# Kernel optimization log

Measured on AMD Instinct MI355X. Metric: run time of the kernel, lower is better.

The kernel has to match this reference:

```python
import jax, jax.numpy as jnp
import numpy as np
from jax import lax

IMG, P, L, H, D, MLPD, NC, B = 224, 16, 12, 12, 768, 3072, 1000, 32
G = IMG // P          # 14 patches per side
S = G * G + 1         # 197 tokens (class token + patches)
DH = D // H           # 64 head dim
EPS = 1e-6


def setup_inputs() -> dict:
    key = jax.random.key(0)
    ks = jax.random.split(key, 10)
    def nrm(k, shape, s=0.02):
        return jax.random.normal(k, shape, jnp.float32) * s
    return {
        "x": jax.random.normal(ks[0], (B, 3, IMG, IMG), jnp.float32),
        "tangent": jax.random.normal(ks[1], (B, 3, IMG, IMG), jnp.float32),
        "conv_w": nrm(ks[2], (D, 3, P, P)),
        "conv_b": jnp.zeros((D,), jnp.float32),
        "class_token": jnp.zeros((1, 1, D), jnp.float32),
        "pos_emb": nrm(ks[3], (1, S, D)),
        "ln1_g": jnp.ones((L, D), jnp.float32), "ln1_b": jnp.zeros((L, D), jnp.float32),
        "qkv_w": nrm(ks[4], (L, 3 * D, D)), "qkv_b": jnp.zeros((L, 3 * D), jnp.float32),
        "out_w": nrm(ks[5], (L, D, D)), "out_b": jnp.zeros((L, D), jnp.float32),
        "ln2_g": jnp.ones((L, D), jnp.float32), "ln2_b": jnp.zeros((L, D), jnp.float32),
        "fc1_w": nrm(ks[6], (L, MLPD, D)), "fc1_b": jnp.zeros((L, MLPD), jnp.float32),
        "fc2_w": nrm(ks[7], (L, D, MLPD)), "fc2_b": jnp.zeros((L, D), jnp.float32),
        "lnf_g": jnp.ones((D,), jnp.float32), "lnf_b": jnp.zeros((D,), jnp.float32),
        "head_w": nrm(ks[8], (NC, D)), "head_b": jnp.zeros((NC,), jnp.float32),
    }


def _layer_norm(x, g, b):
    mu = jnp.mean(x, -1, keepdims=True)
    var = jnp.mean(jnp.square(x - mu), -1, keepdims=True)
    return (x - mu) * lax.rsqrt(var + EPS) * g + b


def _vit(x, conv_w, conv_b, class_token, pos_emb, ln1_g, ln1_b, qkv_w, qkv_b,
         out_w, out_b, ln2_g, ln2_b, fc1_w, fc1_b, fc2_w, fc2_b, lnf_g, lnf_b,
         head_w, head_b):
    n = x.shape[0]
    # patch embedding == Conv2d(3, D, kernel=P, stride=P)
    xr = x.reshape(n, 3, G, P, G, P)
    tok = jnp.einsum('ncgphq,dcpq->nghd', xr, conv_w).reshape(n, G * G, D) + conv_b
    cls = jnp.broadcast_to(class_token, (n, 1, D))
    z = jnp.concatenate([cls, tok], axis=1) + pos_emb  # [n, S, D]

    def block(z, p):
        l1g, l1b, qw, qb, ow, ob, l2g, l2b, f1w, f1b, f2w, f2b = p
        y = _layer_norm(z, l1g, l1b)
        qkv = jnp.einsum('nsd,ed->nse', y, qw) + qb          # [n,S,3D]
        q, k, v = jnp.split(qkv, 3, axis=-1)
        q = q.reshape(n, S, H, DH).transpose(0, 2, 1, 3)
        k = k.reshape(n, S, H, DH).transpose(0, 2, 1, 3)
        v = v.reshape(n, S, H, DH).transpose(0, 2, 1, 3)
        scores = jnp.einsum('nhqd,nhkd->nhqk', q, k) / jnp.sqrt(jnp.float32(DH))
        a = jax.nn.softmax(scores, axis=-1)
        o = jnp.einsum('nhqk,nhkd->nhqd', a, v).transpose(0, 2, 1, 3).reshape(n, S, D)
        o = jnp.einsum('nsd,ed->nse', o, ow) + ob
        z = z + o
        y2 = _layer_norm(z, l2g, l2b)
        h = jax.nn.gelu(jnp.einsum('nsd,ed->nse', y2, f1w) + f1b, approximate=False)
        z = z + jnp.einsum('nse,de->nsd', h, f2w) + f2b
        return z, None

    z, _ = lax.scan(block, z, (ln1_g, ln1_b, qkv_w, qkv_b, out_w, out_b,
                               ln2_g, ln2_b, fc1_w, fc1_b, fc2_w, fc2_b))
    z = _layer_norm(z, lnf_g, lnf_b)
    return z[:, 0] @ head_w.T + head_b  # [n, NC]


def reference(x, tangent, conv_w, conv_b, class_token, pos_emb, ln1_g, ln1_b,
              qkv_w, qkv_b, out_w, out_b, ln2_g, ln2_b, fc1_w, fc1_b, fc2_w,
              fc2_b, lnf_g, lnf_b, head_w, head_b):
    f = lambda xx: _vit(xx, conv_w, conv_b, class_token, pos_emb, ln1_g, ln1_b,
                        qkv_w, qkv_b, out_w, out_b, ln2_g, ln2_b, fc1_w, fc1_b,
                        fc2_w, fc2_b, lnf_g, lnf_b, head_w, head_b)
    out, out_jvp = jax.jvp(f, (x,), (tangent,))
    return out, out_jvp
```

## Files before the change

kernel.cpp:

```cpp
#include <hip/hip_runtime.h>
#include <math.h>

static constexpr int B_   = 32;
static constexpr int S_   = 197;
static constexpr int D_   = 768;
static constexpr int H_   = 12;
static constexpr int L_   = 12;
static constexpr int MD_  = 3072;
static constexpr int NC_  = 1000;
static constexpr int GP_  = 196;
static constexpr int KP_  = 224;
static constexpr int MP_  = 6400;

typedef __attribute__((ext_vector_type(8))) short bf16x8v;
typedef __attribute__((ext_vector_type(4))) float f32x4v;

__device__ __forceinline__ unsigned short f2bf(float x) {
    union { float f; unsigned u; } v; v.f = x;
    unsigned r = v.u + 0x7fffu + ((v.u >> 16) & 1u);
    return (unsigned short)(r >> 16);
}

#define GLOAD_LDS16(gptr, lptr) \
    __builtin_amdgcn_global_load_lds((const __attribute__((address_space(1))) void*)(gptr), \
        (__attribute__((address_space(3))) void*)(lptr), 16, 0, 0)

template<int MODE, bool BIAS>
__global__ __launch_bounds__(512, 2) void mfma_pair_kernel(
    const short* __restrict__ Af, const short* __restrict__ At,
    const short* __restrict__ Bm, const float* __restrict__ bias,
    void* __restrict__ Cfv, void* __restrict__ Ctv,
    int Mhalf, int N, int K, int ldc)
{
    int bx, by;
    {
        const int gx = gridDim.x, nwg = gx * gridDim.y;
        const int flat = blockIdx.y * gx + blockIdx.x;
        const int q = nwg >> 3, r = nwg & 7;
        const int xcd = flat & 7, idx = flat >> 3;
        const int nf = (xcd < r ? xcd * (q + 1) : r * (q + 1) + (xcd - r) * q) + idx;
        bx = nf % gx; by = nf / gx;
    }
    __shared__ __align__(16) short ldsAf[2][128 * 32];
    __shared__ __align__(16) short ldsAt[2][128 * 32];
    __shared__ __align__(16) short ldsB [2][128 * 32];
    const int tid  = threadIdx.x;
    const int lane = tid & 63;
    const int w    = tid >> 6;
    const int m0 = by * 128, n0 = bx * 128;
    const int wr = w >> 1, wc = w & 1;
    f32x4v accf[2][4] = {}, acct[2][4] = {};

    const int r_in = lane >> 2;
    const int cdst = lane & 3;
    const int srow = w * 16 + r_in;
    const int csrc = cdst ^ ((srow >> 1) & 3);
    const size_t aoff = (size_t)(m0 + srow) * K + csrc * 8;
    const size_t boff = (size_t)(n0 + srow) * K + csrc * 8;

    GLOAD_LDS16(Af + aoff, &ldsAf[0][w * 512]);
    GLOAD_LDS16(At + aoff, &ldsAt[0][w * 512]);
    GLOAD_LDS16(Bm + boff, &ldsB [0][w * 512]);
    __syncthreads();

    int cur = 0;
    for (int k0 = 0; k0 < K; k0 += 32) {
        const int nxt = cur ^ 1;
        if (k0 + 32 < K) {
            GLOAD_LDS16(Af + aoff + k0 + 32, &ldsAf[nxt][w * 512]);
            GLOAD_LDS16(At + aoff + k0 + 32, &ldsAt[nxt][w * 512]);
            GLOAD_LDS16(Bm + boff + k0 + 32, &ldsB [nxt][w * 512]);
        }
        bf16x8v af[2], at[2], bfr[4];
        #pragma unroll
        for (int m = 0; m < 2; ++m) {
            const int row = wr * 32 + m * 16 + (lane & 15);
            const int c = (lane >> 4) ^ ((row >> 1) & 3);
            af[m] = *(const bf16x8v*)&ldsAf[cur][row * 32 + c * 8];
            at[m] = *(const bf16x8v*)&ldsAt[cur][row * 32 + c * 8];
        }
        #pragma unroll
        for (int n = 0; n < 4; ++n) {
            const int row = wc * 64 + n * 16 + (lane & 15);
            const int c = (lane >> 4) ^ ((row >> 1) & 3);
            bfr[n] = *(const bf16x8v*)&ldsB[cur][row * 32 + c * 8];
        }
        #pragma unroll
        for (int m = 0; m < 2; ++m)
            #pragma unroll
            for (int n = 0; n < 4; ++n) {
                accf[m][n] = __builtin_amdgcn_mfma_f32_16x16x32_bf16(af[m], bfr[n], accf[m][n], 0, 0, 0);
                acct[m][n] = __builtin_amdgcn_mfma_f32_16x16x32_bf16(at[m], bfr[n], acct[m][n], 0, 0, 0);
            }
        __syncthreads();
        cur = nxt;
    }
    const int col_base = n0 + wc * 64 + (lane & 15);
    const int row_base = m0 + wr * 32 + (lane >> 4) * 4;
    #pragma unroll
    for (int n = 0; n < 4; ++n) {
        const int col = col_base + n * 16;
        const float bv = BIAS ? bias[col] : 0.f;
        #pragma unroll
        for (int m = 0; m < 2; ++m) {
            const int row = row_base + m * 16;
            #pragma unroll
            for (int r = 0; r < 4; ++r) {
                if (row + r < Mhalf) {
                    const size_t off = (size_t)(row + r) * ldc + col;
                    const float vf = accf[m][n][r] + bv;
                    const float vt = acct[m][n][r];
                    if (MODE == 0) {
                        ((float*)Cfv)[off] = vf;
                        ((float*)Ctv)[off] = vt;
                    } else if (MODE == 1) {
                        ((float*)Cfv)[off] += vf;
                        ((float*)Ctv)[off] += vt;
                    } else if (MODE == 2) {
                        ((short*)Cfv)[off] = (short)f2bf(vf);
                        ((short*)Ctv)[off] = (short)f2bf(vt);
                    } else {
                        const float cdf = 0.5f * (1.0f + erff(vf * 0.70710678118654752f));
                        const float pdf = 0.3989422804014327f * expf(-0.5f * vf * vf);
                        ((short*)Cfv)[off] = (short)f2bf(vf * cdf);
                        ((short*)Ctv)[off] = (short)f2bf(vt * (cdf + vf * pdf));
                    }
                }
            }
        }
    }
}

__global__ __launch_bounds__(256) void attn_fused_kernel(
    const short* __restrict__ qkvb, const short* __restrict__ dqkvb,
    const short* __restrict__ Vtb_, const short* __restrict__ dVtb_,
    short* __restrict__ obf, short* __restrict__ dobf)
{
    const int qt = blockIdx.x;
    const int b  = blockIdx.y;
    const int n = b / H_, h = b - n * H_;
    const short* qb  = qkvb  + (size_t)n * S_ * 2304 + h * 64;
    const short* kb  = qb + 768;
    const short* dqb = dqkvb + (size_t)n * S_ * 2304 + h * 64;
    const short* dkb = dqb + 768;
    const short* Vb  = Vtb_  + (size_t)b * 64 * KP_;
    const short* dVb = dVtb_ + (size_t)b * 64 * KP_;

    __shared__ __align__(16) short lds[32768];
    const int tid = threadIdx.x, lane = tid & 63, w = tid >> 6;
    const int g = lane >> 4, kc = lane & 15;
    const int srow = lane >> 2, cdst = lane & 3;
    const int csrc = cdst ^ ((srow >> 1) & 3);

    {
        const size_t qr = (size_t)min(qt * 64 + w * 16 + srow, S_ - 1) * 2304;
        #pragma unroll
        for (int kw = 0; kw < 2; ++kw) {
            GLOAD_LDS16(qb  + qr + kw * 32 + csrc * 8, &lds[w * 1024 + kw * 512]);
            GLOAD_LDS16(dqb + qr + kw * 32 + csrc * 8, &lds[4096 + w * 1024 + kw * 512]);
        }
    }

    f32x4v aS[14], aD[14];
    #pragma unroll
    for (int i = 0; i < 14; ++i) { aS[i] = (f32x4v){0,0,0,0}; aD[i] = (f32x4v){0,0,0,0}; }
    bf16x8v qf[2], dqf[2];

    #pragma unroll
    for (int kt = 0; kt < 7; ++kt) {
        {
            const int kwin = w & 1;
            const short* src = (w < 2) ? kb : dkb;
            const int base = (w < 2) ? 8192 : 10240;
            #pragma unroll
            for (int half = 0; half < 2; ++half) {
                const size_t kr = (size_t)min(kt * 32 + half * 16 + srow, S_ - 1) * 2304;
                GLOAD_LDS16(src + kr + kwin * 32 + csrc * 8,
                            &lds[base + kwin * 1024 + half * 512]);
            }
        }
        __syncthreads();
        if (kt == 0) {
            #pragma unroll
            for (int kw = 0; kw < 2; ++kw) {
                const int c = g ^ ((kc >> 1) & 3);
                qf[kw]  = *(const bf16x8v*)&lds[w * 1024 + kw * 512 + kc * 32 + c * 8];
                dqf[kw] = *(const bf16x8v*)&lds[4096 + w * 1024 + kw * 512 + kc * 32 + c * 8];
            }
        }
        #pragma unroll
        for (int nf = 0; nf < 2; ++nf) {
            const int row = nf * 16 + kc;
            const int c = g ^ ((row >> 1) & 3);
            const bf16x8v kf0  = *(const bf16x8v*)&lds[8192  + row * 32 + c * 8];
            const bf16x8v kf1  = *(const bf16x8v*)&lds[8192  + 1024 + row * 32 + c * 8];
            const bf16x8v dkf0 = *(const bf16x8v*)&lds[10240 + row * 32 + c * 8];
            const bf16x8v dkf1 = *(const bf16x8v*)&lds[10240 + 1024 + row * 32 + c * 8];
            const int fi = kt * 2 + nf;
            aS[fi] = __builtin_amdgcn_mfma_f32_16x16x32_bf16(qf[0], kf0, aS[fi], 0,0,0);
            aS[fi] = __builtin_amdgcn_mfma_f32_16x16x32_bf16(qf[1], kf1, aS[fi], 0,0,0);
            aD[fi] = __builtin_amdgcn_mfma_f32_16x16x32_bf16(dqf[0], kf0, aD[fi], 0,0,0);
            aD[fi] = __builtin_amdgcn_mfma_f32_16x16x32_bf16(dqf[1], kf1, aD[fi], 0,0,0);
            aD[fi] = __builtin_amdgcn_mfma_f32_16x16x32_bf16(qf[0], dkf0, aD[fi], 0,0,0);
            aD[fi] = __builtin_amdgcn_mfma_f32_16x16x32_bf16(qf[1], dkf1, aD[fi], 0,0,0);
        }
        __syncthreads();
    }

    float pm[4] = {-3.0e38f, -3.0e38f, -3.0e38f, -3.0e38f};
    #pragma unroll
    for (int fi = 0; fi < 14; ++fi) {
        if (fi * 16 + kc < S_) {
            #pragma unroll
            for (int r = 0; r < 4; ++r) pm[r] = fmaxf(pm[r], aS[fi][r]);
        }
    }
    #pragma unroll
    for (int off = 1; off < 16; off <<= 1)
        #pragma unroll
        for (int r = 0; r < 4; ++r) pm[r] = fmaxf(pm[r], __shfl_xor(pm[r], off));

    float den[4] = {0,0,0,0}, tsm[4] = {0,0,0,0};
    #pragma unroll
    for (int fi = 0; fi < 14; ++fi) {
        const bool val = fi * 16 + kc < S_;
        #pragma unroll
        for (int r = 0; r < 4; ++r) {
            const float s  = aS[fi][r] * 0.125f;
            const float ds = aD[fi][r] * 0.125f;
            const float e = val ? expf(s - pm[r] * 0.125f) : 0.f;
            den[r] += e; tsm[r] += e * ds;
            aS[fi][r] = e; aD[fi][r] = ds;
        }
    }
    #pragma unroll
    for (int off = 1; off < 16; off <<= 1)
        #pragma unroll
        for (int r = 0; r < 4; ++r) {
            den[r] += __shfl_xor(den[r], off);
            tsm[r] += __shfl_xor(tsm[r], off);
        }
    float inv[4], tq[4];
    #pragma unroll
    for (int r = 0; r < 4; ++r) { inv[r] = 1.f / den[r]; tq[r] = tsm[r] * inv[r]; }

    const int lpw = w * 3584, ldpw = 14336 + w * 3584;
    #pragma unroll
    for (int fi = 0; fi < 14; ++fi) {
        const int kwin = fi >> 1;
        const int chunkbase = (fi & 1) * 2 + (kc >> 3);
        #pragma unroll
        for (int r = 0; r < 4; ++r) {
            const int qs = g * 4 + r;
            const int swz = chunkbase ^ ((qs >> 1) & 3);
            const int addr = kwin * 512 + qs * 32 + swz * 8 + (kc & 7);
            const float p  = aS[fi][r] * inv[r];
            const float dp = p * (aD[fi][r] - tq[r]);
            lds[lpw  + addr] = (short)f2bf(p);
            lds[ldpw + addr] = (short)f2bf(dp);
        }
    }

    f32x4v aO[4], aDO[4];
    #pragma unroll
    for (int i = 0; i < 4; ++i) { aO[i] = (f32x4v){0,0,0,0}; aDO[i] = (f32x4v){0,0,0,0}; }

    #pragma unroll
    for (int kt = 0; kt < 7; ++kt) {
        {
            const size_t vr = (size_t)(w * 16 + srow) * KP_ + kt * 32 + csrc * 8;
            GLOAD_LDS16(Vb  + vr, &lds[28672 + w * 512]);
            GLOAD_LDS16(dVb + vr, &lds[30720 + w * 512]);
        }
        __syncthreads();
        bf16x8v pa, dpa;
        {
            const int c = g ^ ((kc >> 1) & 3);
            pa  = *(const bf16x8v*)&lds[lpw  + kt * 512 + kc * 32 + c * 8];
            dpa = *(const bf16x8v*)&lds[ldpw + kt * 512 + kc * 32 + c * 8];
        }
        #pragma unroll
        for (int nf = 0; nf < 4; ++nf) {
            const int row = nf * 16 + kc;
            const int c = (g) ^ ((row >> 1) & 3);
            const bf16x8v vf  = *(const bf16x8v*)&lds[28672 + row * 32 + c * 8];
            const bf16x8v dvf = *(const bf16x8v*)&lds[30720 + row * 32 + c * 8];
            aO[nf]  = __builtin_amdgcn_mfma_f32_16x16x32_bf16(pa,  vf,  aO[nf], 0,0,0);
            aDO[nf] = __builtin_amdgcn_mfma_f32_16x16x32_bf16(dpa, vf,  aDO[nf], 0,0,0);
            aDO[nf] = __builtin_amdgcn_mfma_f32_16x16x32_bf16(pa,  dvf, aDO[nf], 0,0,0);
        }
        __syncthreads();
    }

    short* ob  = obf  + (size_t)n * S_ * D_ + h * 64;
    short* dob = dobf + (size_t)n * S_ * D_ + h * 64;
    #pragma unroll
    for (int nf = 0; nf < 4; ++nf) {
        const int dh = nf * 16 + kc;
        #pragma unroll
        for (int r = 0; r < 4; ++r) {
            const int q = qt * 64 + w * 16 + g * 4 + r;
            if (q < S_) {
                ob [(size_t)q * D_ + dh] = (short)f2bf(aO[nf][r]);
                dob[(size_t)q * D_ + dh] = (short)f2bf(aDO[nf][r]);
            }
        }
    }
}

__global__ __launch_bounds__(256) void vtrans_kernel(
    const short* __restrict__ qkvb, const short* __restrict__ dqkvb,
    short* __restrict__ Vt, short* __restrict__ dVt)
{
    const int blk = blockIdx.x;
    const int b = blk >> 2, kt = blk & 3;
    const int n = b / H_, h = b - n * H_;
    const short* vb  = qkvb  + (size_t)n * S_ * 2304 + 1536 + h * 64;
    const short* dvb = dqkvb + (size_t)n * S_ * 2304 + 1536 + h * 64;
    __shared__ short t1[64][65], t2[64][65];
    const int tid = threadIdx.x;
    #pragma unroll
    for (int j = 0; j < 16; ++j) {
        const int e = tid + 256 * j;
        const int kk = e >> 6, dh = e & 63;
        const int gk = kt * 64 + kk;
        short v = 0, dv = 0;
        if (gk < S_) { v = vb[(size_t)gk * 2304 + dh]; dv = dvb[(size_t)gk * 2304 + dh]; }
        t1[dh][kk] = v; t2[dh][kk] = dv;
    }
    __syncthreads();
    #pragma unroll
    for (int j = 0; j < 16; ++j) {
        const int e = tid + 256 * j;
        const int dh = e >> 6, kk = e & 63;
        const int ok = kt * 64 + kk;
        if (ok < KP_) {
            Vt [(size_t)b * 64 * KP_ + (size_t)dh * KP_ + ok] = t1[dh][kk];
            dVt[(size_t)b * 64 * KP_ + (size_t)dh * KP_ + ok] = t2[dh][kk];
        }
    }
}

template<bool BIAS>
__global__ __launch_bounds__(256) void gemm_kernel(
    const float* __restrict__ A, const float* __restrict__ Bm,
    const float* __restrict__ bias, float* __restrict__ C,
    int M, int N, int K, int lda, int ldb, int ldc)
{
    const int tile_m = blockIdx.y * 64, tile_n = blockIdx.x * 64;
    __shared__ float As[16][64];
    __shared__ float Bs[16][64];
    const int tid = threadIdx.x;
    const int tx = tid & 15, ty = tid >> 4;
    float acc[4][4] = {};
    for (int k0 = 0; k0 < K; k0 += 16) {
        {
            const int row = tid >> 2, kc = (tid & 3) * 4, gm = tile_m + row;
            #pragma unroll
            for (int i = 0; i < 4; ++i) {
                const int gk = k0 + kc + i;
                float v = 0.f;
                if (gm < M && gk < K) v = A[(long long)gm * lda + gk];
                As[kc + i][row] = v;
            }
        }
        {
            const int row = tid >> 2, kc = (tid & 3) * 4, gn = tile_n + row;
            #pragma unroll
            for (int i = 0; i < 4; ++i) {
                const int gk = k0 + kc + i;
                float v = 0.f;
                if (gn < N && gk < K) v = Bm[(long long)gn * ldb + gk];
                Bs[kc + i][row] = v;
            }
        }
        __syncthreads();
        #pragma unroll
        for (int kk = 0; kk < 16; ++kk) {
            float a[4], bb[4];
            #pragma unroll
            for (int i = 0; i < 4; ++i) a[i] = As[kk][ty * 4 + i];
            #pragma unroll
            for (int j = 0; j < 4; ++j) bb[j] = Bs[kk][tx * 4 + j];
            #pragma unroll
            for (int i = 0; i < 4; ++i)
                #pragma unroll
                for (int j = 0; j < 4; ++j)
                    acc[i][j] += a[i] * bb[j];
        }
        __syncthreads();
    }
    #pragma unroll
    for (int i = 0; i < 4; ++i) {
        const int gm = tile_m + ty * 4 + i;
        if (gm >= M) continue;
        #pragma unroll
        for (int j = 0; j < 4; ++j) {
            const int gn = tile_n + tx * 4 + j;
            if (gn >= N) continue;
            float v = acc[i][j];
            if (BIAS) v += bias[gn];
            C[(long long)gm * ldc + gn] = v;
        }
    }
}

__device__ __forceinline__ float blk_sum4(float v, float* smem) {
    #pragma unroll
    for (int off = 32; off > 0; off >>= 1) v += __shfl_down(v, off);
    __syncthreads();
    if ((threadIdx.x & 63) == 0) smem[threadIdx.x >> 6] = v;
    __syncthreads();
    return smem[0] + smem[1] + smem[2] + smem[3];
}

template<bool WF32>
__global__ __launch_bounds__(256) void ln_jvp_kernel(
    const float* __restrict__ z, const float* __restrict__ dz,
    const float* __restrict__ g, const float* __restrict__ b,
    float* __restrict__ y, float* __restrict__ dy,
    short* __restrict__ ybf, short* __restrict__ dybf)
{
    const long long row = blockIdx.x;
    const float* xr  = z  + row * D_;
    const float* dxr = dz + row * D_;
    __shared__ float smem[4];
    const int t = threadIdx.x;
    float x[3], dx[3];
    #pragma unroll
    for (int i = 0; i < 3; ++i) { x[i] = xr[t + 256 * i]; dx[i] = dxr[t + 256 * i]; }
    float sx  = blk_sum4(x[0] + x[1] + x[2], smem);
    float sdx = blk_sum4(dx[0] + dx[1] + dx[2], smem);
    const float mu = sx / D_, dmu = sdx / D_;
    float sv = 0.f, sc = 0.f;
    #pragma unroll
    for (int i = 0; i < 3; ++i) {
        const float xc = x[i] - mu;
        sv += xc * xc;
        sc += xc * (dx[i] - dmu);
    }
    sv = blk_sum4(sv, smem);
    sc = blk_sum4(sc, smem);
    const float rstd = rsqrtf(sv / D_ + 1e-6f);
    const float k2   = (sc / D_) * rstd * rstd;
    #pragma unroll
    for (int i = 0; i < 3; ++i) {
        const int c = t + 256 * i;
        const float yh  = (x[i] - mu) * rstd;
        const float dyh = (dx[i] - dmu) * rstd - yh * k2;
        const float yv  = yh * g[c] + b[c];
        const float dyv = dyh * g[c];
        if (WF32) { y[row * D_ + c] = yv; dy[row * D_ + c] = dyv; }
        ybf[row * D_ + c]  = (short)f2bf(yv);
        dybf[row * D_ + c] = (short)f2bf(dyv);
    }
}

__global__ __launch_bounds__(256) void cast_bf16_kernel(
    const float* __restrict__ in, short* __restrict__ out, int n4)
{
    for (int i = blockIdx.x * blockDim.x + threadIdx.x; i < n4;
         i += gridDim.x * blockDim.x) {
        const float4 v = ((const float4*)in)[i];
        short o[4];
        o[0] = (short)f2bf(v.x); o[1] = (short)f2bf(v.y);
        o[2] = (short)f2bf(v.z); o[3] = (short)f2bf(v.w);
        *(short4*)&out[i * 4] = *(short4*)o;
    }
}

__global__ __launch_bounds__(256) void wcast_kernel(
    const float* __restrict__ qw, const float* __restrict__ ow,
    const float* __restrict__ f1, const float* __restrict__ f2,
    short* __restrict__ dq, short* __restrict__ dow,
    short* __restrict__ d1, short* __restrict__ d2)
{
    const int b1 = 442368;
    const int b2 = b1 + 147456;
    const int b3 = b2 + 589824;
    const int total = b3 + 589824;
    for (int i = blockIdx.x * blockDim.x + threadIdx.x; i < total;
         i += gridDim.x * blockDim.x) {
        const float* s; short* d; int j;
        if (i < b1)      { s = qw; d = dq;  j = i; }
        else if (i < b2) { s = ow; d = dow; j = i - b1; }
        else if (i < b3) { s = f1; d = d1;  j = i - b2; }
        else             { s = f2; d = d2;  j = i - b3; }
        const float4 v = ((const float4*)s)[j];
        short o[4];
        o[0] = (short)f2bf(v.x); o[1] = (short)f2bf(v.y);
        o[2] = (short)f2bf(v.z); o[3] = (short)f2bf(v.w);
        *(short4*)&d[j * 4] = *(short4*)o;
    }
}

__global__ __launch_bounds__(256) void im2col_kernel(
    const float* __restrict__ x, short* __restrict__ xp, int total)
{
    for (int i = blockIdx.x * blockDim.x + threadIdx.x; i < total;
         i += gridDim.x * blockDim.x) {
        const int k  = i % 768;
        const int m  = i / 768;
        const int gh = m % GP_;
        const int n  = m / GP_;
        const int q  = k & 15;
        const int p  = (k >> 4) & 15;
        const int c  = k >> 8;
        const int hc = gh % 14, gr = gh / 14;
        const int ir = gr * 16 + p, ic = hc * 16 + q;
        xp[i] = (short)f2bf(x[(((long long)n * 3 + c) * 224 + ir) * 224 + ic]);
    }
}

__global__ __launch_bounds__(256) void assemble_kernel(
    const float* __restrict__ tok, const float* __restrict__ dtok,
    float* __restrict__ z, float* __restrict__ dz,
    const float* __restrict__ cls, const float* __restrict__ pos, int total)
{
    for (int i = blockIdx.x * blockDim.x + threadIdx.x; i < total;
         i += gridDim.x * blockDim.x) {
        const int d = i % D_;
        const int s = (i / D_) % S_;
        const int n = i / (D_ * S_);
        if (s == 0) {
            z[i]  = cls[d] + pos[d];
            dz[i] = 0.f;
        } else {
            const long long ti = ((long long)n * GP_ + s - 1) * D_ + d;
            z[i]  = tok[ti]  + pos[s * D_ + d];
            dz[i] = dtok[ti];
        }
    }
}

static inline void mgemm_pair(hipStream_t st, const short* Af, const short* At,
                              const short* Bm, const float* bias,
                              void* Cf, void* Ct, int Mhalf, int N, int K, int ldc,
                              int mode, bool hasbias)
{
    dim3 grid(N / 128, (Mhalf + 127) / 128);
    dim3 blk(512);
#define PK(MD_, BI) mfma_pair_kernel<MD_, BI><<<grid, blk, 0, st>>>(Af, At, Bm, bias, Cf, Ct, Mhalf, N, K, ldc)
    if (mode == 0) { if (hasbias) PK(0, true); else PK(0, false); }
    else if (mode == 1) { if (hasbias) PK(1, true); else PK(1, false); }
    else if (mode == 2) { if (hasbias) PK(2, true); else PK(2, false); }
    else { if (hasbias) PK(3, true); else PK(3, false); }
#undef PK
}

static inline void cast_bf(hipStream_t st, const float* in, short* out, long long n) {
    const int n4 = (int)(n / 4);
    int g = (n4 + 255) / 256; if (g > 4096) g = 4096;
    cast_bf16_kernel<<<g, 256, 0, st>>>(in, out, n4);
}

extern "C" void kernel_launch(void* const* d_in, const int* in_sizes, int n_in,
                              void* d_out, int out_size, void* d_ws, size_t ws_size,
                              hipStream_t stream)
{
    const float* x       = (const float*)d_in[0];
    const float* tangent = (const float*)d_in[1];
    const float* conv_w  = (const float*)d_in[2];
    const float* conv_b  = (const float*)d_in[3];
    const float* cls     = (const float*)d_in[4];
    const float* pos     = (const float*)d_in[5];
    const float* ln1_g   = (const float*)d_in[6];
    const float* ln1_b   = (const float*)d_in[7];
    const float* qkv_w   = (const float*)d_in[8];
    const float* qkv_b   = (const float*)d_in[9];
    const float* out_w   = (const float*)d_in[10];
    const float* out_b   = (const float*)d_in[11];
    const float* ln2_g   = (const float*)d_in[12];
    const float* ln2_b   = (const float*)d_in[13];
    const float* fc1_w   = (const float*)d_in[14];
    const float* fc1_b   = (const float*)d_in[15];
    const float* fc2_w   = (const float*)d_in[16];
    const float* fc2_b   = (const float*)d_in[17];
    const float* lnf_g   = (const float*)d_in[18];
    const float* lnf_b   = (const float*)d_in[19];
    const float* head_w  = (const float*)d_in[20];
    const float* head_b  = (const float*)d_in[21];
    float* out = (float*)d_out;

    const int nBS = B_ * S_;
    const int NB = B_ * H_;
    const long long SD = (long long)S_ * D_;
    const long long PZ = (long long)MP_ * D_;
    const long long PQ = (long long)MP_ * 2304;
    const long long PH = (long long)MP_ * MD_;
    const long long PTOK = (long long)B_ * GP_ * D_;

    float* f = (float*)d_ws;
    float* z     = f;
    float* dz    = z + PZ;
    float* tok   = dz + PZ;
    float* dtok  = tok + PTOK;
    float* yf    = tok;
    float* dyf   = tok + PTOK;
    yf  = tok;
    dyf = tok + PZ;

    short* sh     = (short*)(tok + 2 * PZ);
    short* ybf    = sh;
    short* dybf   = ybf + PZ;
    short* qkvbf  = dybf + PZ;
    short* dqkvbf = qkvbf + PQ;
    short* Vt     = dqkvbf + PQ;
    short* dVt    = Vt + (long long)NB * 64 * KP_;
    short* hbf    = dVt + (long long)NB * 64 * KP_;
    short* dhbf   = hbf + PH;
    short* xpbf   = hbf;
    short* dxpbf  = hbf + PTOK;
    short* wq     = dhbf + PH;
    short* wo     = wq + 2304 * 768;
    short* w1     = wo + 768 * 768;
    short* w2     = w1 + 3072 * 768;
    short* cwbf   = w2 + 768 * 3072;

    {
        const int total = (int)PTOK;
        im2col_kernel<<<8192, 256, 0, stream>>>(x, xpbf, total);
        im2col_kernel<<<8192, 256, 0, stream>>>(tangent, dxpbf, total);
        cast_bf(stream, conv_w, cwbf, 768 * 768);
        mgemm_pair(stream, xpbf, dxpbf, cwbf, conv_b, tok, dtok,
                   B_ * GP_, D_, D_, D_, 0, true);
        const int tz = (int)(B_ * SD);
        assemble_kernel<<<8192, 256, 0, stream>>>(tok, dtok, z, dz, cls, pos, tz);
    }

    for (int l = 0; l < L_; ++l) {
        const float* l1g = ln1_g + (long long)l * D_;
        const float* l1b = ln1_b + (long long)l * D_;
        const float* qb  = qkv_b + (long long)l * 3 * D_;
        const float* ob  = out_b + (long long)l * D_;
        const float* l2g = ln2_g + (long long)l * D_;
        const float* l2b = ln2_b + (long long)l * D_;
        const float* f1b = fc1_b + (long long)l * MD_;
        const float* f2b = fc2_b + (long long)l * D_;

        wcast_kernel<<<4096, 256, 0, stream>>>(
            qkv_w + (long long)l * 3 * D_ * D_, out_w + (long long)l * D_ * D_,
            fc1_w + (long long)l * MD_ * D_,    fc2_w + (long long)l * D_ * MD_,
            wq, wo, w1, w2);

        ln_jvp_kernel<false><<<nBS, 256, 0, stream>>>(z, dz, l1g, l1b, nullptr, nullptr, ybf, dybf);
        mgemm_pair(stream, ybf, dybf, wq, qb, qkvbf, dqkvbf,
                   nBS, 3 * D_, D_, 3 * D_, 2, true);

        vtrans_kernel<<<NB * 4, 256, 0, stream>>>(qkvbf, dqkvbf, Vt, dVt);
        attn_fused_kernel<<<dim3(4, NB), 256, 0, stream>>>(qkvbf, dqkvbf, Vt, dVt, ybf, dybf);

        mgemm_pair(stream, ybf, dybf, wo, ob, z, dz, nBS, D_, D_, D_, 1, true);

        ln_jvp_kernel<false><<<nBS, 256, 0, stream>>>(z, dz, l2g, l2b, nullptr, nullptr, ybf, dybf);
        mgemm_pair(stream, ybf, dybf, w1, f1b, hbf, dhbf, nBS, MD_, D_, MD_, 3, true);
        mgemm_pair(stream, hbf, dhbf, w2, f2b, z, dz, nBS, D_, MD_, D_, 1, true);
    }

    ln_jvp_kernel<true><<<nBS, 256, 0, stream>>>(z, dz, lnf_g, lnf_b, yf, dyf, ybf, dybf);
    gemm_kernel<true><<<dim3((NC_ + 63) / 64, 1), 256, 0, stream>>>(
        yf,  head_w, head_b, out,            B_, NC_, D_, (int)SD, D_, NC_);
    gemm_kernel<false><<<dim3((NC_ + 63) / 64, 1), 256, 0, stream>>>(
        dyf, head_w, nullptr, out + B_ * NC_, B_, NC_, D_, (int)SD, D_, NC_);
}
```

Before: 5.081 ms.

## Triple-buffer LDS in paired MFMA GEMM with explicit vmcnt waits

Expands the GEMM's LDS staging from two buffers to three and prefetches two k-steps ahead using direct global-to-LDS loads. The per-iteration __syncthreads is replaced by a targeted s_waitcnt vmcnt plus s_barrier, so only the oldest stage must land before compute. This aims to hide global memory latency better. The cost is more LDS per block, which could limit occupancy, and reliance on hand-counted vmcnt.

Measured after the change: 5.184 ms. 1.02x slower.

```diff
diff --git a/kernel.cpp b/kernel.cpp
--- a/kernel.cpp
+++ b/kernel.cpp
@@ -41,9 +41,9 @@
         const int nf = (xcd < r ? xcd * (q + 1) : r * (q + 1) + (xcd - r) * q) + idx;
         bx = nf % gx; by = nf / gx;
     }
-    __shared__ __align__(16) short ldsAf[2][128 * 32];
-    __shared__ __align__(16) short ldsAt[2][128 * 32];
-    __shared__ __align__(16) short ldsB [2][128 * 32];
+    __shared__ __align__(16) short ldsAf[3][128 * 32];
+    __shared__ __align__(16) short ldsAt[3][128 * 32];
+    __shared__ __align__(16) short ldsB [3][128 * 32];
     const int tid  = threadIdx.x;
     const int lane = tid & 63;
     const int w    = tid >> 6;
@@ -58,32 +58,39 @@
     const size_t aoff = (size_t)(m0 + srow) * K + csrc * 8;
     const size_t boff = (size_t)(n0 + srow) * K + csrc * 8;
 
-    GLOAD_LDS16(Af + aoff, &ldsAf[0][w * 512]);
-    GLOAD_LDS16(At + aoff, &ldsAt[0][w * 512]);
-    GLOAD_LDS16(Bm + boff, &ldsB [0][w * 512]);
-    __syncthreads();
-
-    int cur = 0;
-    for (int k0 = 0; k0 < K; k0 += 32) {
-        const int nxt = cur ^ 1;
-        if (k0 + 32 < K) {
-            GLOAD_LDS16(Af + aoff + k0 + 32, &ldsAf[nxt][w * 512]);
-            GLOAD_LDS16(At + aoff + k0 + 32, &ldsAt[nxt][w * 512]);
-            GLOAD_LDS16(Bm + boff + k0 + 32, &ldsB [nxt][w * 512]);
-        }
+    const int NSTEP = K >> 5;
+#define STAGE(step) do {                                                        \
+        if ((step) < NSTEP) {                                                   \
+            const int _b = (step) % 3;                                          \
+            GLOAD_LDS16(Af + aoff + (size_t)(step) * 32, &ldsAf[_b][w * 512]);  \
+            GLOAD_LDS16(At + aoff + (size_t)(step) * 32, &ldsAt[_b][w * 512]);  \
+            GLOAD_LDS16(Bm + boff + (size_t)(step) * 32, &ldsB [_b][w * 512]);  \
+        } } while (0)
+
+    STAGE(0);
+    STAGE(1);
+    if (NSTEP > 1) asm volatile("s_waitcnt vmcnt(3)" ::: "memory");
+    else           asm volatile("s_waitcnt vmcnt(0)" ::: "memory");
+    __builtin_amdgcn_s_barrier();
+    __builtin_amdgcn_sched_barrier(0);
+
+    for (int k = 0; k < NSTEP; ++k) {
+        STAGE(k + 2);
+        __builtin_amdgcn_sched_barrier(0);
+        const int cb = k % 3;
         bf16x8v af[2], at[2], bfr[4];
         #pragma unroll
         for (int m = 0; m < 2; ++m) {
             const int row = wr * 32 + m * 16 + (lane & 15);
             const int c = (lane >> 4) ^ ((row >> 1) & 3);
-            af[m] = *(const bf16x8v*)&ldsAf[cur][row * 32 + c * 8];
-            at[m] = *(const bf16x8v*)&ldsAt[cur][row * 32 + c * 8];
+            af[m] = *(const bf16x8v*)&ldsAf[cb][row * 32 + c * 8];
+            at[m] = *(const bf16x8v*)&ldsAt[cb][row * 32 + c * 8];
         }
         #pragma unroll
         for (int n = 0; n < 4; ++n) {
             const int row = wc * 64 + n * 16 + (lane & 15);
             const int c = (lane >> 4) ^ ((row >> 1) & 3);
-            bfr[n] = *(const bf16x8v*)&ldsB[cur][row * 32 + c * 8];
+            bfr[n] = *(const bf16x8v*)&ldsB[cb][row * 32 + c * 8];
         }
         #pragma unroll
         for (int m = 0; m < 2; ++m)
@@ -92,9 +99,13 @@
                 accf[m][n] = __builtin_amdgcn_mfma_f32_16x16x32_bf16(af[m], bfr[n], accf[m][n], 0, 0, 0);
                 acct[m][n] = __builtin_amdgcn_mfma_f32_16x16x32_bf16(at[m], bfr[n], acct[m][n], 0, 0, 0);
             }
-        __syncthreads();
-        cur = nxt;
-    }
+        if (k + 2 < NSTEP) asm volatile("s_waitcnt vmcnt(3)" ::: "memory");
+        else               asm volatile("s_waitcnt vmcnt(0)" ::: "memory");
+        __builtin_amdgcn_s_barrier();
+        __builtin_amdgcn_sched_barrier(0);
+    }
+#undef STAGE
+
     const int col_base = n0 + wc * 64 + (lane & 15);
     const int row_base = m0 + wr * 32 + (lane >> 4) * 4;
     #pragma unroll
@@ -596,9 +607,7 @@
     float* tok   = dz + PZ;
     float* dtok  = tok + PTOK;
     float* yf    = tok;
-    float* dyf   = tok + PTOK;
-    yf  = tok;
-    dyf = tok + PZ;
+    float* dyf   = tok + PZ;
 
     short* sh     = (short*)(tok + 2 * PZ);
     short* ybf    = sh;
```

## Load A operands directly from global into registers in paired MFMA GEMM

Applied to the files above, without the earlier changes.

The paired primal/tangent GEMM kernel no longer stages the A and At tiles through LDS. Each wave now loads its own A fragments straight from global memory into registers, software-prefetched one K-step ahead, while only B still goes through double-buffered LDS. This cuts LDS footprint and LDS traffic and may allow more occupancy. In exchange it issues uncoalesced per-lane 16-byte global loads, and rows shared by the two column waves are fetched twice. The epilogue and swizzle are factored into helpers and a redundant pointer assignment is removed.

Result: slower. 7.784 ms (+53.2%).

```diff
diff --git a/kernel.cpp b/kernel.cpp
--- a/kernel.cpp
+++ b/kernel.cpp
@@ -25,6 +25,35 @@
     __builtin_amdgcn_global_load_lds((const __attribute__((address_space(1))) void*)(gptr), \
         (__attribute__((address_space(3))) void*)(lptr), 16, 0, 0)
 
+__device__ __forceinline__ void xcd_swizzle(int& bx, int& by) {
+    const int gx = gridDim.x, nwg = gx * gridDim.y;
+    const int flat = blockIdx.y * gx + blockIdx.x;
+    const int q = nwg >> 3, r = nwg & 7;
+    const int xcd = flat & 7, idx = flat >> 3;
+    const int nf = (xcd < r ? xcd * (q + 1) : r * (q + 1) + (xcd - r) * q) + idx;
+    bx = nf % gx; by = nf / gx;
+}
+
+template<int MODE>
+__device__ __forceinline__ void pair_store(void* Cfv, void* Ctv, size_t off,
+                                           float vf, float vt) {
+    if (MODE == 0) {
+        ((float*)Cfv)[off] = vf;
+        ((float*)Ctv)[off] = vt;
+    } else if (MODE == 1) {
+        ((float*)Cfv)[off] += vf;
+        ((float*)Ctv)[off] += vt;
+    } else if (MODE == 2) {
+        ((short*)Cfv)[off] = (short)f2bf(vf);
+        ((short*)Ctv)[off] = (short)f2bf(vt);
+    } else {
+        const float cdf = 0.5f * (1.0f + erff(vf * 0.70710678118654752f));
+        const float pdf = 0.3989422804014327f * expf(-0.5f * vf * vf);
+        ((short*)Cfv)[off] = (short)f2bf(vf * cdf);
+        ((short*)Ctv)[off] = (short)f2bf(vt * (cdf + vf * pdf));
+    }
+}
+
 template<int MODE, bool BIAS>
 __global__ __launch_bounds__(512, 2) void mfma_pair_kernel(
     const short* __restrict__ Af, const short* __restrict__ At,
@@ -32,18 +61,8 @@
     void* __restrict__ Cfv, void* __restrict__ Ctv,
     int Mhalf, int N, int K, int ldc)
 {
-    int bx, by;
-    {
-        const int gx = gridDim.x, nwg = gx * gridDim.y;
-        const int flat = blockIdx.y * gx + blockIdx.x;
-        const int q = nwg >> 3, r = nwg & 7;
-        const int xcd = flat & 7, idx = flat >> 3;
-        const int nf = (xcd < r ? xcd * (q + 1) : r * (q + 1) + (xcd - r) * q) + idx;
-        bx = nf % gx; by = nf / gx;
-    }
-    __shared__ __align__(16) short ldsAf[2][128 * 32];
-    __shared__ __align__(16) short ldsAt[2][128 * 32];
-    __shared__ __align__(16) short ldsB [2][128 * 32];
+    int bx, by; xcd_swizzle(bx, by);
+    __shared__ __align__(16) short ldsB[2][128 * 32];
     const int tid  = threadIdx.x;
     const int lane = tid & 63;
     const int w    = tid >> 6;
@@ -55,34 +74,42 @@
     const int cdst = lane & 3;
     const int srow = w * 16 + r_in;
     const int csrc = cdst ^ ((srow >> 1) & 3);
-    const size_t aoff = (size_t)(m0 + srow) * K + csrc * 8;
     const size_t boff = (size_t)(n0 + srow) * K + csrc * 8;
 
-    GLOAD_LDS16(Af + aoff, &ldsAf[0][w * 512]);
-    GLOAD_LDS16(At + aoff, &ldsAt[0][w * 512]);
-    GLOAD_LDS16(Bm + boff, &ldsB [0][w * 512]);
+    const int g = lane >> 4;
+    size_t aoffm[2];
+    #pragma unroll
+    for (int m = 0; m < 2; ++m)
+        aoffm[m] = (size_t)(m0 + wr * 32 + m * 16 + (lane & 15)) * K + g * 8;
+
+    GLOAD_LDS16(Bm + boff, &ldsB[0][w * 512]);
+    bf16x8v af[2], at[2];
+    #pragma unroll
+    for (int m = 0; m < 2; ++m) {
+        af[m] = *(const bf16x8v*)(Af + aoffm[m]);
+        at[m] = *(const bf16x8v*)(At + aoffm[m]);
+    }
     __syncthreads();
 
+    const int NSTEP = K >> 5;
     int cur = 0;
-    for (int k0 = 0; k0 < K; k0 += 32) {
+    for (int k = 0; k < NSTEP; ++k) {
         const int nxt = cur ^ 1;
-        if (k0 + 32 < K) {
-            GLOAD_LDS16(Af + aoff + k0 + 32, &ldsAf[nxt][w * 512]);
-            GLOAD_LDS16(At + aoff + k0 + 32, &ldsAt[nxt][w * 512]);
-            GLOAD_LDS16(Bm + boff + k0 + 32, &ldsB [nxt][w * 512]);
-        }
-        bf16x8v af[2], at[2], bfr[4];
-        #pragma unroll
-        for (int m = 0; m < 2; ++m) {
-            const int row = wr * 32 + m * 16 + (lane & 15);
-            const int c = (lane >> 4) ^ ((row >> 1) & 3);
-            af[m] = *(const bf16x8v*)&ldsAf[cur][row * 32 + c * 8];
-            at[m] = *(const bf16x8v*)&ldsAt[cur][row * 32 + c * 8];
-        }
+        bf16x8v afn[2], atn[2];
+        if (k + 1 < NSTEP) {
+            const size_t kk = (size_t)(k + 1) * 32;
+            GLOAD_LDS16(Bm + boff + kk, &ldsB[nxt][w * 512]);
+            #pragma unroll
+            for (int m = 0; m < 2; ++m) {
+                afn[m] = *(const bf16x8v*)(Af + aoffm[m] + kk);
+                atn[m] = *(const bf16x8v*)(At + aoffm[m] + kk);
+            }
+        }
+        bf16x8v bfr[4];
         #pragma unroll
         for (int n = 0; n < 4; ++n) {
             const int row = wc * 64 + n * 16 + (lane & 15);
-            const int c = (lane >> 4) ^ ((row >> 1) & 3);
+            const int c = g ^ ((row >> 1) & 3);
             bfr[n] = *(const bf16x8v*)&ldsB[cur][row * 32 + c * 8];
         }
         #pragma unroll
@@ -93,8 +120,11 @@
                 acct[m][n] = __builtin_amdgcn_mfma_f32_16x16x32_bf16(at[m], bfr[n], acct[m][n], 0, 0, 0);
             }
         __syncthreads();
+        #pragma unroll
+        for (int m = 0; m < 2; ++m) { af[m] = afn[m]; at[m] = atn[m]; }
         cur = nxt;
     }
+
     const int col_base = n0 + wc * 64 + (lane & 15);
     const int row_base = m0 + wr * 32 + (lane >> 4) * 4;
     #pragma unroll
@@ -108,23 +138,7 @@
             for (int r = 0; r < 4; ++r) {
                 if (row + r < Mhalf) {
                     const size_t off = (size_t)(row + r) * ldc + col;
-                    const float vf = accf[m][n][r] + bv;
-                    const float vt = acct[m][n][r];
-                    if (MODE == 0) {
-                        ((float*)Cfv)[off] = vf;
-                        ((float*)Ctv)[off] = vt;
-                    } else if (MODE == 1) {
-                        ((float*)Cfv)[off] += vf;
-                        ((float*)Ctv)[off] += vt;
-                    } else if (MODE == 2) {
-                        ((short*)Cfv)[off] = (short)f2bf(vf);
-                        ((short*)Ctv)[off] = (short)f2bf(vt);
-                    } else {
-                        const float cdf = 0.5f * (1.0f + erff(vf * 0.70710678118654752f));
-                        const float pdf = 0.3989422804014327f * expf(-0.5f * vf * vf);
-                        ((short*)Cfv)[off] = (short)f2bf(vf * cdf);
-                        ((short*)Ctv)[off] = (short)f2bf(vt * (cdf + vf * pdf));
-                    }
+                    pair_store<MODE>(Cfv, Ctv, off, accf[m][n][r] + bv, acct[m][n][r]);
                 }
             }
         }
@@ -596,9 +610,7 @@
     float* tok   = dz + PZ;
     float* dtok  = tok + PTOK;
     float* yf    = tok;
-    float* dyf   = tok + PTOK;
-    yf  = tok;
-    dyf = tok + PZ;
+    float* dyf   = tok + PZ;
 
     short* sh     = (short*)(tok + 2 * PZ);
     short* ybf    = sh;
```
